# Optimization experiments

Measured on AMD Instinct MI355X. Metric: run time of the kernel, lower is better.

## Reference

```python
import jax, jax.numpy as jnp
import numpy as np

B, T, V, D, N = 32, 15, 100, 768, 160
ANGLE_POS = 7  # angle_feat_size + 3
MAX_STEPS = 100
LN_EPS = 1e-12


def setup_inputs() -> dict:
    key = jax.random.key(0)
    ks = jax.random.split(key, 10)
    split_traj_embeds = jax.random.normal(ks[0], (B, T, V, D), jnp.float32)
    gmap_pos_fts = jax.random.normal(ks[1], (B, N, ANGLE_POS), jnp.float32)
    step_emb_table = jax.random.normal(ks[2], (MAX_STEPS, D), jnp.float32) * 0.02
    pos_w = jax.random.normal(ks[3], (ANGLE_POS, D), jnp.float32) * 0.02
    pos_b = jnp.zeros((D,), jnp.float32)
    ln_g = jnp.ones((D,), jnp.float32)
    ln_b = jnp.zeros((D,), jnp.float32)
    # view lengths in [1, V]
    split_traj_vp_lens = jax.random.randint(ks[4], (B, T), 1, V + 1, jnp.int32)
    # each step visits a distinct node id t+1 (node 0 is the null/stop node)
    traj_vpids = jnp.tile(jnp.arange(1, T + 1, dtype=jnp.int32)[None, :], (B, 1))
    traj_cand_vpids = jax.random.randint(ks[5], (B, T, V), 0, N, jnp.int32)
    gmap_step_ids = jax.random.randint(ks[6], (B, N), 0, MAX_STEPS, jnp.int32)
    gmap_lens = jax.random.randint(ks[7], (B,), N // 2, N + 1, jnp.int32)
    return {
        "split_traj_embeds": split_traj_embeds,
        "gmap_pos_fts": gmap_pos_fts,
        "step_emb_table": step_emb_table,
        "pos_w": pos_w,
        "pos_b": pos_b,
        "ln_g": ln_g,
        "ln_b": ln_b,
        "split_traj_vp_lens": split_traj_vp_lens,
        "traj_vpids": traj_vpids,
        "traj_cand_vpids": traj_cand_vpids,
        "gmap_step_ids": gmap_step_ids,
        "gmap_lens": gmap_lens,
    }


def _layer_norm(x, g, b):
    mu = jnp.mean(x, axis=-1, keepdims=True)
    var = jnp.mean(jnp.square(x - mu), axis=-1, keepdims=True)
    return (x - mu) / jnp.sqrt(var + LN_EPS) * g + b


def reference(split_traj_embeds, gmap_pos_fts, step_emb_table, pos_w, pos_b,
              ln_g, ln_b, split_traj_vp_lens, traj_vpids, traj_cand_vpids,
              gmap_step_ids, gmap_lens):
    b, t, v, d = split_traj_embeds.shape
    n = gmap_step_ids.shape[1]
    # view validity mask per step: [B,T,V]
    vmask = (jnp.arange(v)[None, None, :] < split_traj_vp_lens[:, :, None])
    emb = split_traj_embeds * vmask[..., None].astype(split_traj_embeds.dtype)
    # visited-node feature: masked mean over views at each step -> [B,T,D]
    visited_feat = jnp.sum(emb, axis=2) / split_traj_vp_lens[..., None].astype(emb.dtype)
    # scatter visited features to node slots (distinct ids per batch)
    flat_vis_ids = (jnp.arange(b, dtype=jnp.int32)[:, None] * n + traj_vpids).reshape(-1)
    visited = jnp.zeros((b * n, d), emb.dtype).at[flat_vis_ids].set(visited_feat.reshape(-1, d))
    visited_mask = jnp.zeros((b * n,), emb.dtype).at[flat_vis_ids].set(1.0)
    # unvisited-node feature: mean over all candidate view features per node
    flat_cand_ids = (jnp.arange(b, dtype=jnp.int32)[:, None, None] * n + traj_cand_vpids).reshape(-1)
    cand_feats = emb.reshape(-1, d)
    cand_valid = vmask.reshape(-1).astype(emb.dtype)
    seg_sum = jax.ops.segment_sum(cand_feats * cand_valid[:, None], flat_cand_ids, num_segments=b * n)
    seg_cnt = jax.ops.segment_sum(cand_valid, flat_cand_ids, num_segments=b * n)
    cand_mean = seg_sum / jnp.maximum(seg_cnt, 1.0)[:, None]
    # visited takes precedence over candidate mean (matches final gather in torch code)
    gmap_img = jnp.where(visited_mask[:, None] > 0, visited, cand_mean).reshape(b, n, d)
    # node 0 is the null/stop token -> zero row (torch cat of zeros)
    gmap_img = gmap_img.at[:, 0].set(0.0)
    step_emb = step_emb_table[gmap_step_ids]                      # [B,N,D]
    pos_emb = _layer_norm(gmap_pos_fts @ pos_w + pos_b, ln_g, ln_b)  # [B,N,D]
    gmap_embeds = gmap_img + step_emb + pos_emb
    return gmap_embeds
```

## Files before the change

kernel.cpp:

```cpp
#include <hip/hip_runtime.h>

constexpr int cB = 32, cT = 15, cV = 100, cD = 768, cN = 160, cAP = 7;
constexpr int cD4 = cD / 4;
constexpr int cTV = cT * cV;
constexpr float cLN_EPS = 1e-12f;

__global__ __launch_bounds__(192) void k_all(
    const float4* __restrict__ emb,
    const float*  __restrict__ pos_fts,
    const float4* __restrict__ step_tab,
    const float4* __restrict__ pos_w,
    const float4* __restrict__ pos_b,
    const float4* __restrict__ ln_g,
    const float4* __restrict__ ln_b,
    const int*    __restrict__ vp_lens,
    const int*    __restrict__ vpids,
    const int*    __restrict__ cand_ids,
    const int*    __restrict__ step_ids,
    float4*       __restrict__ out)
{
    const int n   = blockIdx.x;
    const int b   = blockIdx.y;
    const int row = b * cN + n;
    const int tid = threadIdx.x;

    __shared__ float sf[cAP];
    __shared__ int   slen[cT];
    __shared__ int   svp[cT];
    __shared__ float red[8];
    __shared__ int   scount;
    __shared__ int   slist[cTV];

    if (tid < cAP) sf[tid] = pos_fts[row * cAP + tid];
    if (tid >= 32 && tid < 32 + cT) slen[tid - 32] = vp_lens[b * cT + (tid - 32)];
    if (tid >= 64 && tid < 64 + cT) svp[tid - 64]  = vpids[b * cT + (tid - 64)];
    if (tid == 0) scount = 0;
    __syncthreads();

    float4 x = pos_b[tid];
#pragma unroll
    for (int k = 0; k < cAP; ++k) {
        const float4 w = pos_w[k * cD4 + tid];
        const float f = sf[k];
        x.x = fmaf(f, w.x, x.x); x.y = fmaf(f, w.y, x.y);
        x.z = fmaf(f, w.z, x.z); x.w = fmaf(f, w.w, x.w);
    }
    float s  = x.x + x.y + x.z + x.w;
    float ss = x.x * x.x + x.y * x.y + x.z * x.z + x.w * x.w;
    for (int off = 32; off; off >>= 1) {
        s  += __shfl_down(s,  off, 64);
        ss += __shfl_down(ss, off, 64);
    }
    const int wid = tid >> 6, lane = tid & 63;
    if (lane == 0) { red[wid * 2] = s; red[wid * 2 + 1] = ss; }
    __syncthreads();
    if (tid == 0) {
        float S = 0.f, SS = 0.f;
        for (int w = 0; w < 3; ++w) { S += red[w * 2]; SS += red[w * 2 + 1]; }
        const float mu  = S / (float)cD;
        const float var = SS / (float)cD - mu * mu;
        red[6] = mu;
        red[7] = rsqrtf(fmaxf(var, 0.f) + cLN_EPS);
    }
    __syncthreads();
    const float mu = red[6], rs = red[7];

    float ax = 0.f, ay = 0.f, az = 0.f, aw = 0.f;
    float wgt = 0.f;
    if (n > 0) {
        int tvis = -1;
#pragma unroll
        for (int k = cT - 1; k >= 0; --k) if (tvis < 0 && svp[k] == n) tvis = k;
        if (tvis >= 0) {
            const int bt  = b * cT + tvis;
            const int len = slen[tvis];
            const float4* base = emb + (size_t)bt * cV * cD4 + tid;
            int i = 0;
            for (; i + 4 <= len; i += 4) {
                const float4 a0 = base[(size_t)(i + 0) * cD4];
                const float4 a1 = base[(size_t)(i + 1) * cD4];
                const float4 a2 = base[(size_t)(i + 2) * cD4];
                const float4 a3 = base[(size_t)(i + 3) * cD4];
                ax += (a0.x + a1.x) + (a2.x + a3.x);
                ay += (a0.y + a1.y) + (a2.y + a3.y);
                az += (a0.z + a1.z) + (a2.z + a3.z);
                aw += (a0.w + a1.w) + (a2.w + a3.w);
            }
            for (; i < len; ++i) {
                const float4 a0 = base[(size_t)i * cD4];
                ax += a0.x; ay += a0.y; az += a0.z; aw += a0.w;
            }
            wgt = 1.0f / (float)len;
        } else {
            const int* cb = cand_ids + (size_t)b * cTV;
            for (int e = tid; e < cTV; e += 192) {
                const int t = e / cV;
                const int v = e - t * cV;
                if (v < slen[t] && cb[e] == n) {
                    const int p = atomicAdd(&scount, 1);
                    slist[p] = e;
                }
            }
            __syncthreads();
            const int m = scount;
            const float4* base = emb + (size_t)b * cTV * cD4 + tid;
            int j = 0;
            for (; j + 4 <= m; j += 4) {
                const float4 a0 = base[(size_t)slist[j + 0] * cD4];
                const float4 a1 = base[(size_t)slist[j + 1] * cD4];
                const float4 a2 = base[(size_t)slist[j + 2] * cD4];
                const float4 a3 = base[(size_t)slist[j + 3] * cD4];
                ax += (a0.x + a1.x) + (a2.x + a3.x);
                ay += (a0.y + a1.y) + (a2.y + a3.y);
                az += (a0.z + a1.z) + (a2.z + a3.z);
                aw += (a0.w + a1.w) + (a2.w + a3.w);
            }
            for (; j < m; ++j) {
                const float4 a0 = base[(size_t)slist[j] * cD4];
                ax += a0.x; ay += a0.y; az += a0.z; aw += a0.w;
            }
            if (m > 0) wgt = 1.0f / (float)m;
        }
    }

    const int sid = step_ids[row];
    const float4 se = step_tab[(size_t)sid * cD4 + tid];
    const float4 g  = ln_g[tid];
    const float4 bb = ln_b[tid];
    float4 o;
    o.x = (x.x - mu) * rs * g.x + bb.x + se.x + ax * wgt;
    o.y = (x.y - mu) * rs * g.y + bb.y + se.y + ay * wgt;
    o.z = (x.z - mu) * rs * g.z + bb.z + se.z + az * wgt;
    o.w = (x.w - mu) * rs * g.w + bb.w + se.w + aw * wgt;
    out[(size_t)row * cD4 + tid] = o;
}

extern "C" void kernel_launch(void* const* d_in, const int* in_sizes, int n_in,
                              void* d_out, int out_size, void* d_ws, size_t ws_size,
                              hipStream_t stream) {
    const float* emb      = (const float*)d_in[0];
    const float* pos_fts  = (const float*)d_in[1];
    const float* step_tab = (const float*)d_in[2];
    const float* pos_w    = (const float*)d_in[3];
    const float* pos_b    = (const float*)d_in[4];
    const float* ln_g     = (const float*)d_in[5];
    const float* ln_b     = (const float*)d_in[6];
    const int*   vp_lens  = (const int*)d_in[7];
    const int*   vpids    = (const int*)d_in[8];
    const int*   cand     = (const int*)d_in[9];
    const int*   step_ids = (const int*)d_in[10];

    dim3 grid(cN, cB);
    k_all<<<grid, 192, 0, stream>>>((const float4*)emb, pos_fts,
                                    (const float4*)step_tab,
                                    (const float4*)pos_w, (const float4*)pos_b,
                                    (const float4*)ln_g, (const float4*)ln_b,
                                    vp_lens, vpids, cand, step_ids,
                                    (float4*)d_out);
}
```

Measured before the change: 36.98 us.

## Split view gather across two thread groups and vectorize candidate scan

Doubles the block to 384 threads so two groups of 192 each sum half of the gathered view rows, then combines the partial sums through shared memory. The candidate-id scan now uses int4 loads from 375 threads and runs before the LayerNorm reduction, so the gather and the position projection can overlap. The gather loop is unrolled by 8 with clamped, masked loads to raise memory-level parallelism. In exchange it adds an extra shared-memory buffer, wasted loads in the tail iterations, and a larger block that may lower occupancy.

```diff
diff --git a/kernel.cpp b/kernel.cpp
--- a/kernel.cpp
+++ b/kernel.cpp
@@ -5,7 +5,7 @@
 constexpr int cTV = cT * cV;
 constexpr float cLN_EPS = 1e-12f;
 
-__global__ __launch_bounds__(192) void k_all(
+__global__ __launch_bounds__(384) void k_all(
     const float4* __restrict__ emb,
     const float*  __restrict__ pos_fts,
     const float4* __restrict__ step_tab,
@@ -23,13 +23,15 @@
     const int b   = blockIdx.y;
     const int row = b * cN + n;
     const int tid = threadIdx.x;
+    const int grp  = (tid >= 192) ? 1 : 0;
+    const int slot = tid - (grp ? 192 : 0);
 
-    __shared__ float sf[cAP];
-    __shared__ int   slen[cT];
-    __shared__ int   svp[cT];
-    __shared__ float red[8];
-    __shared__ int   scount;
-    __shared__ int   slist[cTV];
+    __shared__ float  sf[cAP];
+    __shared__ int    slen[cT], svp[cT];
+    __shared__ float  red[8];
+    __shared__ int    scount;
+    __shared__ int    slist[cTV];
+    __shared__ float4 spart[192];
 
     if (tid < cAP) sf[tid] = pos_fts[row * cAP + tid];
     if (tid >= 32 && tid < 32 + cT) slen[tid - 32] = vp_lens[b * cT + (tid - 32)];
@@ -37,102 +39,117 @@
     if (tid == 0) scount = 0;
     __syncthreads();
 
-    float4 x = pos_b[tid];
+    int tvis = -1;
 #pragma unroll
-    for (int k = 0; k < cAP; ++k) {
-        const float4 w = pos_w[k * cD4 + tid];
-        const float f = sf[k];
-        x.x = fmaf(f, w.x, x.x); x.y = fmaf(f, w.y, x.y);
-        x.z = fmaf(f, w.z, x.z); x.w = fmaf(f, w.w, x.w);
+    for (int k = cT - 1; k >= 0; --k) if (tvis < 0 && svp[k] == n) tvis = k;
+
+    const bool isCand = (n > 0) && (tvis < 0);
+    if (isCand && tid < cTV / 4) {
+        const int4 c4 = ((const int4*)(cand_ids + (size_t)b * cTV))[tid];
+        const int e0 = tid * 4;
+        const int cc[4] = {c4.x, c4.y, c4.z, c4.w};
+#pragma unroll
+        for (int k = 0; k < 4; ++k) {
+            const int e = e0 + k;
+            const int t = e / cV;
+            const int v = e - t * cV;
+            if (cc[k] == n && v < slen[t]) slist[atomicAdd(&scount, 1)] = e;
+        }
     }
-    float s  = x.x + x.y + x.z + x.w;
-    float ss = x.x * x.x + x.y * x.y + x.z * x.z + x.w * x.w;
-    for (int off = 32; off; off >>= 1) {
-        s  += __shfl_down(s,  off, 64);
-        ss += __shfl_down(ss, off, 64);
+    __syncthreads();
+
+    float4 x = make_float4(0.f, 0.f, 0.f, 0.f);
+    if (!grp) {
+        x = pos_b[slot];
+#pragma unroll
+        for (int k = 0; k < cAP; ++k) {
+            const float4 w = pos_w[k * cD4 + slot];
+            const float f = sf[k];
+            x.x = fmaf(f, w.x, x.x); x.y = fmaf(f, w.y, x.y);
+            x.z = fmaf(f, w.z, x.z); x.w = fmaf(f, w.w, x.w);
+        }
     }
-    const int wid = tid >> 6, lane = tid & 63;
-    if (lane == 0) { red[wid * 2] = s; red[wid * 2 + 1] = ss; }
+
+    float ax = 0.f, ay = 0.f, az = 0.f, aw = 0.f;
+    float wgt = 0.f;
+    if (n > 0) {
+        if (tvis >= 0) {
+            const int len  = slen[tvis];
+            const int half = (len + 1) >> 1;
+            const int i0 = grp ? half : 0;
+            const int i1 = grp ? len  : half;
+            const float4* base = emb + (size_t)(b * cT + tvis) * cV * cD4 + slot;
+            for (int i = i0; i < i1; i += 8) {
+#pragma unroll
+                for (int k = 0; k < 8; ++k) {
+                    const int ik = min(i + k, i1 - 1);
+                    const float4 a0 = base[(size_t)ik * cD4];
+                    const float mk = (i + k < i1) ? 1.f : 0.f;
+                    ax = fmaf(a0.x, mk, ax); ay = fmaf(a0.y, mk, ay);
+                    az = fmaf(a0.z, mk, az); aw = fmaf(a0.w, mk, aw);
+                }
+            }
+            wgt = 1.0f / (float)len;
+        } else {
+            const int m = scount;
+            if (m > 0) {
+                const int half = (m + 1) >> 1;
+                const int j0 = grp ? half : 0;
+                const int j1 = grp ? m    : half;
+                const float4* base = emb + (size_t)b * cTV * cD4 + slot;
+                for (int j = j0; j < j1; j += 8) {
+#pragma unroll
+                    for (int k = 0; k < 8; ++k) {
+                        const int jk = min(j + k, j1 - 1);
+                        const float4 a0 = base[(size_t)slist[jk] * cD4];
+                        const float mk = (j + k < j1) ? 1.f : 0.f;
+                        ax = fmaf(a0.x, mk, ax); ay = fmaf(a0.y, mk, ay);
+                        az = fmaf(a0.z, mk, az); aw = fmaf(a0.w, mk, aw);
+                    }
+                }
+                wgt = 1.0f / (float)m;
+            }
+        }
+    }
+
+    if (grp) spart[slot] = make_float4(ax, ay, az, aw);
+
+    float s = 0.f, ss = 0.f;
+    if (!grp) {
+        s  = x.x + x.y + x.z + x.w;
+        ss = x.x * x.x + x.y * x.y + x.z * x.z + x.w * x.w;
+        for (int off = 32; off; off >>= 1) {
+            s  += __shfl_down(s,  off, 64);
+            ss += __shfl_down(ss, off, 64);
+        }
+        if ((tid & 63) == 0) { red[(tid >> 6) * 2] = s; red[(tid >> 6) * 2 + 1] = ss; }
+    }
     __syncthreads();
     if (tid == 0) {
-        float S = 0.f, SS = 0.f;
-        for (int w = 0; w < 3; ++w) { S += red[w * 2]; SS += red[w * 2 + 1]; }
+        const float S  = red[0] + red[2] + red[4];
+        const float SS = red[1] + red[3] + red[5];
         const float mu  = S / (float)cD;
         const float var = SS / (float)cD - mu * mu;
         red[6] = mu;
         red[7] = rsqrtf(fmaxf(var, 0.f) + cLN_EPS);
     }
     __syncthreads();
-    const float mu = red[6], rs = red[7];
 
-    float ax = 0.f, ay = 0.f, az = 0.f, aw = 0.f;
-    float wgt = 0.f;
-    if (n > 0) {
-        int tvis = -1;
-#pragma unroll
-        for (int k = cT - 1; k >= 0; --k) if (tvis < 0 && svp[k] == n) tvis = k;
-        if (tvis >= 0) {
-            const int bt  = b * cT + tvis;
-            const int len = slen[tvis];
-            const float4* base = emb + (size_t)bt * cV * cD4 + tid;
-            int i = 0;
-            for (; i + 4 <= len; i += 4) {
-                const float4 a0 = base[(size_t)(i + 0) * cD4];
-                const float4 a1 = base[(size_t)(i + 1) * cD4];
-                const float4 a2 = base[(size_t)(i + 2) * cD4];
-                const float4 a3 = base[(size_t)(i + 3) * cD4];
-                ax += (a0.x + a1.x) + (a2.x + a3.x);
-                ay += (a0.y + a1.y) + (a2.y + a3.y);
-                az += (a0.z + a1.z) + (a2.z + a3.z);
-                aw += (a0.w + a1.w) + (a2.w + a3.w);
-            }
-            for (; i < len; ++i) {
-                const float4 a0 = base[(size_t)i * cD4];
-                ax += a0.x; ay += a0.y; az += a0.z; aw += a0.w;
-            }
-            wgt = 1.0f / (float)len;
-        } else {
-            const int* cb = cand_ids + (size_t)b * cTV;
-            for (int e = tid; e < cTV; e += 192) {
-                const int t = e / cV;
-                const int v = e - t * cV;
-                if (v < slen[t] && cb[e] == n) {
-                    const int p = atomicAdd(&scount, 1);
-                    slist[p] = e;
-                }
-            }
-            __syncthreads();
-            const int m = scount;
-            const float4* base = emb + (size_t)b * cTV * cD4 + tid;
-            int j = 0;
-            for (; j + 4 <= m; j += 4) {
-                const float4 a0 = base[(size_t)slist[j + 0] * cD4];
-                const float4 a1 = base[(size_t)slist[j + 1] * cD4];
-                const float4 a2 = base[(size_t)slist[j + 2] * cD4];
-                const float4 a3 = base[(size_t)slist[j + 3] * cD4];
-                ax += (a0.x + a1.x) + (a2.x + a3.x);
-                ay += (a0.y + a1.y) + (a2.y + a3.y);
-                az += (a0.z + a1.z) + (a2.z + a3.z);
-                aw += (a0.w + a1.w) + (a2.w + a3.w);
-            }
-            for (; j < m; ++j) {
-                const float4 a0 = base[(size_t)slist[j] * cD4];
-                ax += a0.x; ay += a0.y; az += a0.z; aw += a0.w;
-            }
-            if (m > 0) wgt = 1.0f / (float)m;
-        }
+    if (!grp) {
+        const float mu = red[6], rs = red[7];
+        const float4 p = spart[slot];
+        ax += p.x; ay += p.y; az += p.z; aw += p.w;
+        const int sid = step_ids[row];
+        const float4 se = step_tab[(size_t)sid * cD4 + slot];
+        const float4 g  = ln_g[slot];
+        const float4 bb = ln_b[slot];
+        float4 o;
+        o.x = (x.x - mu) * rs * g.x + bb.x + se.x + ax * wgt;
+        o.y = (x.y - mu) * rs * g.y + bb.y + se.y + ay * wgt;
+        o.z = (x.z - mu) * rs * g.z + bb.z + se.z + az * wgt;
+        o.w = (x.w - mu) * rs * g.w + bb.w + se.w + aw * wgt;
+        out[(size_t)row * cD4 + slot] = o;
     }
-
-    const int sid = step_ids[row];
-    const float4 se = step_tab[(size_t)sid * cD4 + tid];
-    const float4 g  = ln_g[tid];
-    const float4 bb = ln_b[tid];
-    float4 o;
-    o.x = (x.x - mu) * rs * g.x + bb.x + se.x + ax * wgt;
-    o.y = (x.y - mu) * rs * g.y + bb.y + se.y + ay * wgt;
-    o.z = (x.z - mu) * rs * g.z + bb.z + se.z + az * wgt;
-    o.w = (x.w - mu) * rs * g.w + bb.w + se.w + aw * wgt;
-    out[(size_t)row * cD4 + tid] = o;
 }
 
 extern "C" void kernel_launch(void* const* d_in, const int* in_sizes, int n_in,
@@ -151,7 +168,7 @@
     const int*   step_ids = (const int*)d_in[10];
 
     dim3 grid(cN, cB);
-    k_all<<<grid, 192, 0, stream>>>((const float4*)emb, pos_fts,
+    k_all<<<grid, 384, 0, stream>>>((const float4*)emb, pos_fts,
                                     (const float4*)step_tab,
                                     (const float4*)pos_w, (const float4*)pos_b,
                                     (const float4*)ln_g, (const float4*)ln_b,
```

Result: slower. 38.44 us (+4.0%).

## Split visited-node view reduction across extra blocks and add fixup kernel

Applied to the files above, without the earlier changes.

The long serial reduction over up to 100 views for visited nodes is split into four quarters. The main block sums the first quarter, and 45 extra blocks per batch sum the other three quarters into workspace. A second small kernel adds those partial sums, scaled by 1/len, into the output rows of visited nodes. The candidate scan also moves before the layer-norm computation and uses int4 loads. The aim is to shorten the critical path set by the slowest blocks, at the cost of a second launch, a workspace round trip and a read-modify-write of the visited output rows.

```diff
diff --git a/kernel.cpp b/kernel.cpp
--- a/kernel.cpp
+++ b/kernel.cpp
@@ -3,9 +3,10 @@
 constexpr int cB = 32, cT = 15, cV = 100, cD = 768, cN = 160, cAP = 7;
 constexpr int cD4 = cD / 4;
 constexpr int cTV = cT * cV;
+constexpr int cXB = 3 * cT;
 constexpr float cLN_EPS = 1e-12f;
 
-__global__ __launch_bounds__(192) void k_all(
+__global__ __launch_bounds__(192) void k_main(
     const float4* __restrict__ emb,
     const float*  __restrict__ pos_fts,
     const float4* __restrict__ step_tab,
@@ -17,25 +18,78 @@
     const int*    __restrict__ vpids,
     const int*    __restrict__ cand_ids,
     const int*    __restrict__ step_ids,
+    float4*       __restrict__ wsv,
     float4*       __restrict__ out)
 {
-    const int n   = blockIdx.x;
+    const int nb  = blockIdx.x;
     const int b   = blockIdx.y;
-    const int row = b * cN + n;
     const int tid = threadIdx.x;
 
     __shared__ float sf[cAP];
-    __shared__ int   slen[cT];
-    __shared__ int   svp[cT];
+    __shared__ int   slen[cT], svp[cT];
     __shared__ float red[8];
     __shared__ int   scount;
     __shared__ int   slist[cTV];
 
-    if (tid < cAP) sf[tid] = pos_fts[row * cAP + tid];
-    if (tid >= 32 && tid < 32 + cT) slen[tid - 32] = vp_lens[b * cT + (tid - 32)];
-    if (tid >= 64 && tid < 64 + cT) svp[tid - 64]  = vpids[b * cT + (tid - 64)];
+    if (tid < cT) slen[tid] = vp_lens[b * cT + tid];
+    if (tid >= 32 && tid < 32 + cT) svp[tid - 32] = vpids[b * cT + (tid - 32)];
+
+    if (nb >= cN) {
+        __syncthreads();
+        const int j = nb - cN;
+        const int t = j / 3;
+        const int q = j - t * 3 + 1;
+        const int len = slen[t];
+        const int lo = (len * q) >> 2;
+        const int hi = (len * (q + 1)) >> 2;
+        float ax = 0.f, ay = 0.f, az = 0.f, aw = 0.f;
+        const float4* base = emb + (size_t)(b * cT + t) * cV * cD4 + tid;
+        int i = lo;
+        for (; i + 4 <= hi; i += 4) {
+            const float4 a0 = base[(size_t)(i + 0) * cD4];
+            const float4 a1 = base[(size_t)(i + 1) * cD4];
+            const float4 a2 = base[(size_t)(i + 2) * cD4];
+            const float4 a3 = base[(size_t)(i + 3) * cD4];
+            ax += (a0.x + a1.x) + (a2.x + a3.x);
+            ay += (a0.y + a1.y) + (a2.y + a3.y);
+            az += (a0.z + a1.z) + (a2.z + a3.z);
+            aw += (a0.w + a1.w) + (a2.w + a3.w);
+        }
+        for (; i < hi; ++i) {
+            const float4 a0 = base[(size_t)i * cD4];
+            ax += a0.x; ay += a0.y; az += a0.z; aw += a0.w;
+        }
+        wsv[(size_t)((b * cT + t) * 3 + (q - 1)) * cD4 + tid] =
+            make_float4(ax, ay, az, aw);
+        return;
+    }
+
+    const int n   = nb;
+    const int row = b * cN + n;
+    if (tid >= 64 && tid < 64 + cAP) sf[tid - 64] = pos_fts[row * cAP + (tid - 64)];
     if (tid == 0) scount = 0;
     __syncthreads();
+
+    int tvis = -1;
+#pragma unroll
+    for (int k = cT - 1; k >= 0; --k) if (tvis < 0 && svp[k] == n) tvis = k;
+
+    const bool isCand = (n > 0) && (tvis < 0);
+    if (isCand) {
+        const int4* cb4 = (const int4*)(cand_ids + (size_t)b * cTV);
+        for (int u = tid; u < cTV / 4; u += 192) {
+            const int4 c4 = cb4[u];
+            const int e0 = u * 4;
+            const int cc[4] = {c4.x, c4.y, c4.z, c4.w};
+#pragma unroll
+            for (int k = 0; k < 4; ++k) {
+                const int e = e0 + k;
+                const int t = e / cV;
+                const int v = e - t * cV;
+                if (cc[k] == n && v < slen[t]) slist[atomicAdd(&scount, 1)] = e;
+            }
+        }
+    }
 
     float4 x = pos_b[tid];
 #pragma unroll
@@ -51,12 +105,11 @@
         s  += __shfl_down(s,  off, 64);
         ss += __shfl_down(ss, off, 64);
     }
-    const int wid = tid >> 6, lane = tid & 63;
-    if (lane == 0) { red[wid * 2] = s; red[wid * 2 + 1] = ss; }
+    if ((tid & 63) == 0) { red[(tid >> 6) * 2] = s; red[(tid >> 6) * 2 + 1] = ss; }
     __syncthreads();
     if (tid == 0) {
-        float S = 0.f, SS = 0.f;
-        for (int w = 0; w < 3; ++w) { S += red[w * 2]; SS += red[w * 2 + 1]; }
+        const float S  = red[0] + red[2] + red[4];
+        const float SS = red[1] + red[3] + red[5];
         const float mu  = S / (float)cD;
         const float var = SS / (float)cD - mu * mu;
         red[6] = mu;
@@ -68,15 +121,12 @@
     float ax = 0.f, ay = 0.f, az = 0.f, aw = 0.f;
     float wgt = 0.f;
     if (n > 0) {
-        int tvis = -1;
-#pragma unroll
-        for (int k = cT - 1; k >= 0; --k) if (tvis < 0 && svp[k] == n) tvis = k;
         if (tvis >= 0) {
-            const int bt  = b * cT + tvis;
             const int len = slen[tvis];
-            const float4* base = emb + (size_t)bt * cV * cD4 + tid;
+            const int hi  = len >> 2;
+            const float4* base = emb + (size_t)(b * cT + tvis) * cV * cD4 + tid;
             int i = 0;
-            for (; i + 4 <= len; i += 4) {
+            for (; i + 4 <= hi; i += 4) {
                 const float4 a0 = base[(size_t)(i + 0) * cD4];
                 const float4 a1 = base[(size_t)(i + 1) * cD4];
                 const float4 a2 = base[(size_t)(i + 2) * cD4];
@@ -86,40 +136,33 @@
                 az += (a0.z + a1.z) + (a2.z + a3.z);
                 aw += (a0.w + a1.w) + (a2.w + a3.w);
             }
-            for (; i < len; ++i) {
+            for (; i < hi; ++i) {
                 const float4 a0 = base[(size_t)i * cD4];
                 ax += a0.x; ay += a0.y; az += a0.z; aw += a0.w;
             }
             wgt = 1.0f / (float)len;
         } else {
-            const int* cb = cand_ids + (size_t)b * cTV;
-            for (int e = tid; e < cTV; e += 192) {
-                const int t = e / cV;
-                const int v = e - t * cV;
-                if (v < slen[t] && cb[e] == n) {
-                    const int p = atomicAdd(&scount, 1);
-                    slist[p] = e;
-                }
-            }
             __syncthreads();
             const int m = scount;
-            const float4* base = emb + (size_t)b * cTV * cD4 + tid;
-            int j = 0;
-            for (; j + 4 <= m; j += 4) {
-                const float4 a0 = base[(size_t)slist[j + 0] * cD4];
-                const float4 a1 = base[(size_t)slist[j + 1] * cD4];
-                const float4 a2 = base[(size_t)slist[j + 2] * cD4];
-                const float4 a3 = base[(size_t)slist[j + 3] * cD4];
-                ax += (a0.x + a1.x) + (a2.x + a3.x);
-                ay += (a0.y + a1.y) + (a2.y + a3.y);
-                az += (a0.z + a1.z) + (a2.z + a3.z);
-                aw += (a0.w + a1.w) + (a2.w + a3.w);
-            }
-            for (; j < m; ++j) {
-                const float4 a0 = base[(size_t)slist[j] * cD4];
-                ax += a0.x; ay += a0.y; az += a0.z; aw += a0.w;
-            }
-            if (m > 0) wgt = 1.0f / (float)m;
+            if (m > 0) {
+                const float4* base = emb + (size_t)b * cTV * cD4 + tid;
+                int j = 0;
+                for (; j + 4 <= m; j += 4) {
+                    const float4 a0 = base[(size_t)slist[j + 0] * cD4];
+                    const float4 a1 = base[(size_t)slist[j + 1] * cD4];
+                    const float4 a2 = base[(size_t)slist[j + 2] * cD4];
+                    const float4 a3 = base[(size_t)slist[j + 3] * cD4];
+                    ax += (a0.x + a1.x) + (a2.x + a3.x);
+                    ay += (a0.y + a1.y) + (a2.y + a3.y);
+                    az += (a0.z + a1.z) + (a2.z + a3.z);
+                    aw += (a0.w + a1.w) + (a2.w + a3.w);
+                }
+                for (; j < m; ++j) {
+                    const float4 a0 = base[(size_t)slist[j] * cD4];
+                    ax += a0.x; ay += a0.y; az += a0.z; aw += a0.w;
+                }
+                wgt = 1.0f / (float)m;
+            }
         }
     }
 
@@ -133,6 +176,32 @@
     o.z = (x.z - mu) * rs * g.z + bb.z + se.z + az * wgt;
     o.w = (x.w - mu) * rs * g.w + bb.w + se.w + aw * wgt;
     out[(size_t)row * cD4 + tid] = o;
+}
+
+__global__ __launch_bounds__(192) void k_fix(
+    const int*    __restrict__ vp_lens,
+    const int*    __restrict__ vpids,
+    const float4* __restrict__ wsv,
+    float4*       __restrict__ out)
+{
+    const int t = blockIdx.x;
+    const int b = blockIdx.y;
+    const int node = vpids[b * cT + t];
+    if (node <= 0 || node >= cN) return;
+    const int len = vp_lens[b * cT + t];
+    const int tid = threadIdx.x;
+    const size_t sbase = (size_t)((b * cT + t) * 3) * cD4 + tid;
+    const float4 p0 = wsv[sbase];
+    const float4 p1 = wsv[sbase + cD4];
+    const float4 p2 = wsv[sbase + 2 * cD4];
+    const float w = 1.0f / (float)len;
+    const size_t orow = (size_t)(b * cN + node) * cD4 + tid;
+    float4 o = out[orow];
+    o.x += ((p0.x + p1.x) + p2.x) * w;
+    o.y += ((p0.y + p1.y) + p2.y) * w;
+    o.z += ((p0.z + p1.z) + p2.z) * w;
+    o.w += ((p0.w + p1.w) + p2.w) * w;
+    out[orow] = o;
 }
 
 extern "C" void kernel_launch(void* const* d_in, const int* in_sizes, int n_in,
@@ -150,11 +219,15 @@
     const int*   cand     = (const int*)d_in[9];
     const int*   step_ids = (const int*)d_in[10];
 
-    dim3 grid(cN, cB);
-    k_all<<<grid, 192, 0, stream>>>((const float4*)emb, pos_fts,
-                                    (const float4*)step_tab,
-                                    (const float4*)pos_w, (const float4*)pos_b,
-                                    (const float4*)ln_g, (const float4*)ln_b,
-                                    vp_lens, vpids, cand, step_ids,
-                                    (float4*)d_out);
+    float4* wsv = (float4*)d_ws;
+
+    dim3 g1(cN + cXB, cB);
+    k_main<<<g1, 192, 0, stream>>>((const float4*)emb, pos_fts,
+                                   (const float4*)step_tab,
+                                   (const float4*)pos_w, (const float4*)pos_b,
+                                   (const float4*)ln_g, (const float4*)ln_b,
+                                   vp_lens, vpids, cand, step_ids,
+                                   wsv, (float4*)d_out);
+    dim3 g2(cT, cB);
+    k_fix<<<g2, 192, 0, stream>>>(vp_lens, vpids, wsv, (float4*)d_out);
 }
```

Result: faster. 31.86 us (-13.9%).
